# Optimization experiments

Measured on AMD Instinct MI355X. Metric: run time of the kernel, lower is better.

## Reference

```python
import jax, jax.numpy as jnp
import numpy as np

EPS = 1e-7
LN_EPS = 1e-5

# Lorentz model, points represented by spatial coords x in R^dim; time coord t = sqrt(K + ||x||^2), K = 1/c.

def log_map_zero(x, c):
    K = 1.0 / c
    sqrtK = jnp.sqrt(K)
    xnorm = jnp.linalg.norm(x, axis=-1, keepdims=True)
    t = jnp.sqrt(K + xnorm * xnorm)
    theta = jnp.arccosh(jnp.maximum(t / sqrtK, 1.0 + EPS))
    return sqrtK * theta * x / jnp.maximum(xnorm, EPS)


def exp_map_zero(v, c):
    K = 1.0 / c
    sqrtK = jnp.sqrt(K)
    vnorm = jnp.linalg.norm(v, axis=-1, keepdims=True)
    return sqrtK * jnp.sinh(vnorm / sqrtK) * v / jnp.maximum(vnorm, EPS)


def layer_norm(x, gamma, beta):
    mu = jnp.mean(x, axis=-1, keepdims=True)
    var = jnp.mean((x - mu) ** 2, axis=-1, keepdims=True)
    return (x - mu) * jax.lax.rsqrt(var + LN_EPS) * gamma + beta


def setup_inputs() -> dict:
    key = jax.random.key(0)
    N, D, E, L = 50000, 128, 800000, 2
    ks = jax.random.split(key, 8)
    x_hyp = jax.random.normal(ks[0], (N, D), dtype=jnp.float32)
    edge_index = jax.random.randint(ks[1], (2, E), 0, N, dtype=jnp.int64)
    W = jax.random.normal(ks[2], (L, D, D), dtype=jnp.float32) / np.sqrt(D)
    b = jnp.zeros((L, D), dtype=jnp.float32)
    gamma = jnp.ones((L, D), dtype=jnp.float32)
    beta = jnp.zeros((L, D), dtype=jnp.float32)
    curv = jnp.ones((L,), dtype=jnp.float32)
    return {"x_hyp": x_hyp, "edge_index": edge_index, "W": W, "b": b,
            "gamma": gamma, "beta": beta, "curv": curv}


def reference(x_hyp, edge_index, W, b, gamma, beta, curv):
    N = x_hyp.shape[0]
    L = W.shape[0]
    src, dst = edge_index[0], edge_index[1]
    # in-degree counts for mean aggregation (clamped to avoid div by 0)
    counts = jax.ops.segment_sum(jnp.ones_like(dst, dtype=x_hyp.dtype), dst, num_segments=N)
    counts = jnp.maximum(counts, 1.0)[:, None]
    x = x_hyp
    for l in range(L):
        # curvature treated as constant (torch uses .item())
        c = jax.lax.stop_gradient(jnp.clip(curv[l], 0.1, 10.0))
        x_tan = log_map_zero(x, c)                      # [N, D]
        x_lin = x_tan @ W[l].T + b[l]                   # [N, D]
        msgs = x_lin[src]                               # [E, D] gather
        agg = jax.ops.segment_sum(msgs, dst, num_segments=N) / counts  # scatter-mean
        x_tan_out = layer_norm(x_tan + agg, gamma[l], beta[l])  # dropout in eval mode
        x = exp_map_zero(x_tan_out, c)
    return x
```

## Files before the change

kernel.cpp:

```cpp
#include <hip/hip_runtime.h>
#include <hip/hip_bf16.h>

typedef __attribute__((ext_vector_type(4))) float f32x4;
typedef __attribute__((ext_vector_type(2))) float f32x2;
typedef __attribute__((ext_vector_type(8))) short bf16x8;

constexpr int D = 128;
constexpr int SB = 256;
constexpr int K4CAP = 8192;
#define FEPS 1e-7f
#define FLN_EPS 1e-5f

__device__ __forceinline__ float groupReduceSum16(float x) {
#pragma unroll
  for (int off = 1; off < 16; off <<= 1) x += __shfl_xor(x, off, 64);
  return x;
}

__device__ __forceinline__ unsigned short f2bf(float x) {
  unsigned int u = __float_as_uint(x);
  u += 0x7fffu + ((u >> 16) & 1u);
  return (unsigned short)(u >> 16);
}

__device__ __forceinline__ unsigned int pack2(float a, float b) {
  return (unsigned int)f2bf(a) | ((unsigned int)f2bf(b) << 16);
}

__device__ __forceinline__ f32x2 unp(unsigned int x) {
  f32x2 r;
  r.x = __uint_as_float(x << 16);
  r.y = __uint_as_float(x & 0xffff0000u);
  return r;
}

struct AccSet {
  f32x2 e0, o0, e1, o1;
};

__device__ __forceinline__ void accu(AccSet& s, uint4 u) {
  f32x2 t;
  t.x = __uint_as_float(u.x << 16);
  t.y = __uint_as_float(u.y << 16);
  s.e0 += t;
  t.x = __uint_as_float(u.x);
  t.y = __uint_as_float(u.y);
  s.o0 += t;
  t.x = __uint_as_float(u.z << 16);
  t.y = __uint_as_float(u.w << 16);
  s.e1 += t;
  t.x = __uint_as_float(u.z);
  t.y = __uint_as_float(u.w);
  s.o1 += t;
}


__global__ __launch_bounds__(1024) void k2_scan(int* __restrict__ bh,
                                                int* __restrict__ bucket_base, int NB, int E) {
  __shared__ int bsum[256];
  int tid = threadIdx.x, lane = tid & 63, wv = tid >> 6;
  for (int bin = wv; bin < NB; bin += 16) {
    int carry = 0;
    int* row = bh + bin * SB;
#pragma unroll
    for (int sgm = 0; sgm < 4; ++sgm) {
      int v = row[sgm * 64 + lane];
      int x = v;
#pragma unroll
      for (int off = 1; off < 64; off <<= 1) {
        int t = __shfl_up(x, off, 64);
        if (lane >= off) x += t;
      }
      row[sgm * 64 + lane] = carry + x - v;
      carry += __shfl(x, 63, 64);
    }
    if (lane == 0) bsum[bin] = carry;
  }
  __syncthreads();
  if (wv == 0) {
    int carry = 0;
    for (int base = 0; base < NB; base += 64) {
      int v = (base + lane < NB) ? bsum[base + lane] : 0;
      int x = v;
#pragma unroll
      for (int off = 1; off < 64; off <<= 1) {
        int t = __shfl_up(x, off, 64);
        if (lane >= off) x += t;
      }
      if (base + lane < NB) {
        int excl = carry + x - v;
        bsum[base + lane] = excl;
        bucket_base[base + lane] = excl;
      }
      carry += __shfl(x, 63, 64);
    }
    if (lane == 0) bucket_base[NB] = E;
  }
  __syncthreads();
  for (int bin = wv; bin < NB; bin += 16) {
    int bb = bsum[bin];
    int* row = bh + bin * SB;
    for (int s = lane; s < SB; s += 64) row[s] += bb;
  }
}

__global__ __launch_bounds__(1024) void k3_scatter(const int* __restrict__ src,
                                                   const int* __restrict__ dst,
                                                   const int* __restrict__ bh,
                                                   unsigned int* __restrict__ ebuf, int E,
                                                   int NB, int chunk) {
  __shared__ int base[256];
  __shared__ int cur[256];
  int tid = threadIdx.x;
  if (tid < 256) {
    base[tid] = (tid < NB) ? bh[tid * SB + blockIdx.x] : 0;
    cur[tid] = 0;
  }
  __syncthreads();
  int e0 = blockIdx.x * chunk;
  int e1 = min(e0 + chunk, E);
  for (int e = e0 + tid; e < e1; e += 1024) {
    int d = dst[e];
    int s = src[e];
    int bin = d >> 8;
    int r = atomicAdd(&cur[bin], 1);
    ebuf[base[bin] + r] = (unsigned int)(s & 0xffff) | ((unsigned int)(d & 255) << 16);
  }
}

__global__ __launch_bounds__(1024) void k4_csr(const unsigned int* __restrict__ ebuf,
                                               const int* __restrict__ bucket_base,
                                               int* __restrict__ rowptr,
                                               unsigned short* __restrict__ col, int N, int NB,
                                               int E) {
  __shared__ unsigned int stash[K4CAP];
  __shared__ int hist[256];
  __shared__ int cur[256];
  int b = blockIdx.x, tid = threadIdx.x;
  int e0 = bucket_base[b], e1 = bucket_base[b + 1];
  int cnt = e1 - e0;
  if (tid < 256) {
    hist[tid] = 0;
    cur[tid] = 0;
  }
  __syncthreads();
  for (int i = tid; i < cnt; i += 1024) {
    unsigned int u = ebuf[e0 + i];
    if (i < K4CAP) stash[i] = u;
    atomicAdd(&hist[u >> 16], 1);
  }
  __syncthreads();
  int lane = tid & 63;
  if (tid < 64) {
    int carry = 0;
#pragma unroll
    for (int sgm = 0; sgm < 4; ++sgm) {
      int v = hist[sgm * 64 + lane];
      int x = v;
#pragma unroll
      for (int off = 1; off < 64; off <<= 1) {
        int t = __shfl_up(x, off, 64);
        if (lane >= off) x += t;
      }
      hist[sgm * 64 + lane] = carry + x - v;
      carry += __shfl(x, 63, 64);
    }
  }
  __syncthreads();
  int node0 = b << 8;
  if (tid < 256 && node0 + tid < N) rowptr[node0 + tid] = e0 + hist[tid];
  if (b == 0 && tid == 0) rowptr[N] = E;
  for (int i = tid; i < cnt; i += 1024) {
    unsigned int u = (i < K4CAP) ? stash[i] : ebuf[e0 + i];
    int slot = u >> 16;
    int r = atomicAdd(&cur[slot], 1);
    col[e0 + hist[slot] + r] = (unsigned short)(u & 0xffff);
  }
}


__device__ __forceinline__ void gemm0_body(int gbid, unsigned short* Wlds,
                                           const float* __restrict__ xf,
                                           const float* __restrict__ Wf,
                                           const float* __restrict__ bias,
                                           const float* __restrict__ curv,
                                           unsigned short* __restrict__ xt,
                                           unsigned short* __restrict__ xl, int N) {
  const float* Wp = Wf;
  for (int idx = threadIdx.x; idx < 2048; idx += 1024) {
    int lanei = idx & 63, kbt = idx >> 6;
    int kb = kbt & 3, tcol = kbt >> 2;
    int g = lanei >> 4, r = lanei & 15;
    const float* s = Wp + (size_t)(tcol * 16 + r) * D + kb * 32 + g * 8;
    float4 f0 = *reinterpret_cast<const float4*>(s);
    float4 f1 = *reinterpret_cast<const float4*>(s + 4);
    uint4 u;
    u.x = pack2(f0.x, f0.y);
    u.y = pack2(f0.z, f0.w);
    u.z = pack2(f1.x, f1.y);
    u.w = pack2(f1.z, f1.w);
    *reinterpret_cast<uint4*>(&Wlds[idx * 8]) = u;
  }
  __syncthreads();
  int lane = threadIdx.x & 63;
  int trow = gbid * 16 + (threadIdx.x >> 6);
  int n0 = trow * 16;
  if (n0 >= N) return;
  int g = lane >> 4, r = lane & 15;
  int ar = n0 + r;
  if (ar > N - 1) ar = N - 1;

  bf16x8 af[4];
  float c = fminf(fmaxf(curv[0], 0.1f), 10.0f);
  float K = 1.0f / c, sqrtK = sqrtf(K);
  float4 fa[4][2];
  float ss = 0.f;
#pragma unroll
  for (int kb = 0; kb < 4; ++kb) {
    const float4* xr = reinterpret_cast<const float4*>(xf + (size_t)ar * D + kb * 32 + g * 8);
    fa[kb][0] = xr[0];
    fa[kb][1] = xr[1];
    ss += fa[kb][0].x * fa[kb][0].x + fa[kb][0].y * fa[kb][0].y + fa[kb][0].z * fa[kb][0].z +
          fa[kb][0].w * fa[kb][0].w;
    ss += fa[kb][1].x * fa[kb][1].x + fa[kb][1].y * fa[kb][1].y + fa[kb][1].z * fa[kb][1].z +
          fa[kb][1].w * fa[kb][1].w;
  }
  ss += __shfl_xor(ss, 16, 64);
  ss += __shfl_xor(ss, 32, 64);
  float xnorm = sqrtf(ss);
  float t = sqrtf(K + ss);
  float theta = acoshf(fmaxf(t / sqrtK, 1.0f + FEPS));
  float scale = sqrtK * theta / fmaxf(xnorm, FEPS);
#pragma unroll
  for (int kb = 0; kb < 4; ++kb) {
    union { bf16x8 v; uint4 u; } cv;
    cv.u.x = pack2(fa[kb][0].x * scale, fa[kb][0].y * scale);
    cv.u.y = pack2(fa[kb][0].z * scale, fa[kb][0].w * scale);
    cv.u.z = pack2(fa[kb][1].x * scale, fa[kb][1].y * scale);
    cv.u.w = pack2(fa[kb][1].z * scale, fa[kb][1].w * scale);
    af[kb] = cv.v;
    *reinterpret_cast<uint4*>(xt + (size_t)ar * D + kb * 32 + g * 8) = cv.u;
  }

  int colj = lane & 15, rb = (lane >> 4) * 4;
#pragma unroll
  for (int tcol = 0; tcol < 8; ++tcol) {
    f32x4 acc = {0.f, 0.f, 0.f, 0.f};
#pragma unroll
    for (int kb = 0; kb < 4; ++kb) {
      bf16x8 bfm = *reinterpret_cast<const bf16x8*>(&Wlds[((tcol * 4 + kb) * 64 + lane) * 8]);
      acc = __builtin_amdgcn_mfma_f32_16x16x32_bf16(af[kb], bfm, acc, 0, 0, 0);
    }
    float bv = bias[tcol * 16 + colj];
#pragma unroll
    for (int i = 0; i < 4; ++i) {
      int row = n0 + rb + i;
      if (row < N) xl[(size_t)row * D + tcol * 16 + colj] = f2bf(acc[i] + bv);
    }
  }
}

__global__ __launch_bounds__(1024) void fusedA_kernel(const int* __restrict__ dst,
                                                      int* __restrict__ bh, int E, int NB,
                                                      int chunk, const float* __restrict__ xf,
                                                      const float* __restrict__ Wf,
                                                      const float* __restrict__ bias,
                                                      const float* __restrict__ curv,
                                                      unsigned short* __restrict__ xt,
                                                      unsigned short* __restrict__ xl, int N,
                                                      unsigned short* __restrict__ W16,
                                                      int nconv, int gblocks) {
  __shared__ unsigned short Wlds[128 * 128];
  int bid = blockIdx.x;
  if (bid < SB) {
    int* h = (int*)Wlds;
    int tid = threadIdx.x;
    if (tid < 256) h[tid] = 0;
    __syncthreads();
    int e0 = bid * chunk;
    int e1 = min(e0 + chunk, E);
    for (int e = e0 + tid; e < e1; e += 1024) atomicAdd(&h[dst[e] >> 8], 1);
    __syncthreads();
    if (tid < NB) bh[tid * SB + bid] = h[tid];
  } else if (bid < SB + gblocks) {
    gemm0_body(bid - SB, Wlds, xf, Wf, bias, curv, xt, xl, N);
  } else {
    for (int i = threadIdx.x * 4; i < nconv; i += 4096) {
      float4 f = *reinterpret_cast<const float4*>(Wf + D * D + i);
      uint2 o;
      o.x = pack2(f.x, f.y);
      o.y = pack2(f.z, f.w);
      *reinterpret_cast<uint2*>(W16 + i) = o;
    }
  }
}


template <int MODE>
__global__ __launch_bounds__(256) void agg_kernel(const unsigned short* __restrict__ xl_in,
                                                  unsigned short* __restrict__ xt,
                                                  const int* __restrict__ rowptr,
                                                  const unsigned short* __restrict__ col,
                                                  const float* __restrict__ gamma,
                                                  const float* __restrict__ beta,
                                                  const float* __restrict__ curv, int l,
                                                  const unsigned short* __restrict__ W16n,
                                                  const float* __restrict__ bias,
                                                  unsigned short* __restrict__ xl_out,
                                                  float* __restrict__ out, int N) {
  __shared__ unsigned short xtile[16 * 136];
  int tid = threadIdx.x;
  int lane = tid & 63;
  int gl = lane & 15, g = lane >> 4;
  int wid = tid >> 6;
  int node = blockIdx.x * 16 + wid * 4 + g;
  bool active = node < N;
  int nd = active ? node : N - 1;

  float c = fminf(fmaxf(curv[l], 0.1f), 10.0f);
  float K = 1.0f / c, sqrtK = sqrtf(K);

  int e0 = rowptr[nd], e1 = rowptr[nd + 1];
  int deg = e1 - e0;
  const unsigned short* cb = col + e0;

  AccSet S[4];
#pragma unroll
  for (int j = 0; j < 4; ++j) {
    S[j].e0 = 0.f;
    S[j].o0 = 0.f;
    S[j].e1 = 0.f;
    S[j].o1 = 0.f;
  }

  const uint4* xlp = reinterpret_cast<const uint4*>(xl_in);
  for (int base = 0; base < deg; base += 16) {
    int cidx = (base + gl < deg) ? (int)cb[base + gl] : 0;
    int m = deg - base;
    if (m > 16) m = 16;
    int k = 0;
    for (; k + 8 <= m; k += 8) {
      uint4 u[8];
#pragma unroll
      for (int t = 0; t < 8; ++t) {
        int s = __shfl(cidx, g * 16 + k + t, 64);
        u[t] = xlp[(size_t)s * 16 + gl];
      }
#pragma unroll
      for (int t = 0; t < 8; ++t) accu(S[t & 3], u[t]);
    }
    for (; k + 2 <= m; k += 2) {
      int s0 = __shfl(cidx, g * 16 + k, 64);
      int s1 = __shfl(cidx, g * 16 + k + 1, 64);
      uint4 u0 = xlp[(size_t)s0 * 16 + gl];
      uint4 u1 = xlp[(size_t)s1 * 16 + gl];
      accu(S[0], u0);
      accu(S[1], u1);
    }
    if (k < m) {
      int s0 = __shfl(cidx, g * 16 + k, 64);
      uint4 u0 = xlp[(size_t)s0 * 16 + gl];
      accu(S[0], u0);
    }
  }
  f32x2 E0 = (S[0].e0 + S[1].e0) + (S[2].e0 + S[3].e0);
  f32x2 O0 = (S[0].o0 + S[1].o0) + (S[2].o0 + S[3].o0);
  f32x2 E1 = (S[0].e1 + S[1].e1) + (S[2].e1 + S[3].e1);
  f32x2 O1 = (S[0].o1 + S[1].o1) + (S[2].o1 + S[3].o1);
  float a[8] = {E0.x, O0.x, E0.y, O0.y, E1.x, O1.x, E1.y, O1.y};

  float inv = 1.f / fmaxf((float)deg, 1.f);
  uint4 ut = reinterpret_cast<const uint4*>(xt)[(size_t)nd * 16 + gl];
  f32x2 utv[4];
  utv[0] = unp(ut.x);
  utv[1] = unp(ut.y);
  utv[2] = unp(ut.z);
  utv[3] = unp(ut.w);
  float v[8];
#pragma unroll
  for (int j = 0; j < 4; ++j) {
    v[2 * j] = utv[j].x + a[2 * j] * inv;
    v[2 * j + 1] = utv[j].y + a[2 * j + 1] * inv;
  }

  float s1 = 0.f, s2 = 0.f;
#pragma unroll
  for (int j = 0; j < 8; ++j) {
    s1 += v[j];
    s2 += v[j] * v[j];
  }
  s1 = groupReduceSum16(s1);
  s2 = groupReduceSum16(s2);
  float mu = s1 * (1.f / 128.f);
  float var = fmaxf(s2 * (1.f / 128.f) - mu * mu, 0.f);
  float rstd = rsqrtf(var + FLN_EPS);

  float4 gm0 = *reinterpret_cast<const float4*>(gamma + l * D + gl * 8);
  float4 gm1 = *reinterpret_cast<const float4*>(gamma + l * D + gl * 8 + 4);
  float4 bt0 = *reinterpret_cast<const float4*>(beta + l * D + gl * 8);
  float4 bt1 = *reinterpret_cast<const float4*>(beta + l * D + gl * 8 + 4);
  float y[8];
  y[0] = (v[0] - mu) * rstd * gm0.x + bt0.x;
  y[1] = (v[1] - mu) * rstd * gm0.y + bt0.y;
  y[2] = (v[2] - mu) * rstd * gm0.z + bt0.z;
  y[3] = (v[3] - mu) * rstd * gm0.w + bt0.w;
  y[4] = (v[4] - mu) * rstd * gm1.x + bt1.x;
  y[5] = (v[5] - mu) * rstd * gm1.y + bt1.y;
  y[6] = (v[6] - mu) * rstd * gm1.z + bt1.z;
  y[7] = (v[7] - mu) * rstd * gm1.w + bt1.w;

  float ss = 0.f;
#pragma unroll
  for (int j = 0; j < 8; ++j) ss += y[j] * y[j];
  ss = groupReduceSum16(ss);
  float vn = sqrtf(ss);
  float sc = sqrtK * sinhf(vn / sqrtK) / fmaxf(vn, FEPS);

  if (MODE == 0) {
    if (active) {
      float4 o0, o1;
      o0.x = y[0] * sc;
      o0.y = y[1] * sc;
      o0.z = y[2] * sc;
      o0.w = y[3] * sc;
      o1.x = y[4] * sc;
      o1.y = y[5] * sc;
      o1.z = y[6] * sc;
      o1.w = y[7] * sc;
      float4* op = reinterpret_cast<float4*>(out + (size_t)node * D + gl * 8);
      op[0] = o0;
      op[1] = o1;
    }
  } else {
    float xn = sqrtK * sinhf(vn / sqrtK);
    float c2 = fminf(fmaxf(curv[l + 1], 0.1f), 10.0f);
    float K2 = 1.0f / c2, sqrtK2 = sqrtf(K2);
    float t2 = sqrtf(K2 + xn * xn);
    float theta = acoshf(fmaxf(t2 / sqrtK2, 1.0f + FEPS));
    float sc2 = sqrtK2 * theta / fmaxf(xn, FEPS);
    float st = sc * sc2;
    uint4 w;
    w.x = pack2(y[0] * st, y[1] * st);
    w.y = pack2(y[2] * st, y[3] * st);
    w.z = pack2(y[4] * st, y[5] * st);
    w.w = pack2(y[6] * st, y[7] * st);
    int noderow = wid * 4 + g;
    *reinterpret_cast<uint4*>(&xtile[noderow * 136 + gl * 8]) = w;
    if (active) reinterpret_cast<uint4*>(xt)[(size_t)node * 16 + gl] = w;
    __syncthreads();

    int rr = lane & 15, kg = lane >> 4;
    bf16x8 af[4];
#pragma unroll
    for (int kb = 0; kb < 4; ++kb)
      af[kb] = *reinterpret_cast<const bf16x8*>(&xtile[rr * 136 + kb * 32 + kg * 8]);
    int n0 = blockIdx.x * 16;
    int rb = kg * 4;
#pragma unroll
    for (int t = 0; t < 2; ++t) {
      int tcol = wid * 2 + t;
      f32x4 acc = {0.f, 0.f, 0.f, 0.f};
#pragma unroll
      for (int kb = 0; kb < 4; ++kb) {
        bf16x8 bfm = *reinterpret_cast<const bf16x8*>(W16n + (size_t)(tcol * 16 + rr) * D +
                                                      kb * 32 + kg * 8);
        acc = __builtin_amdgcn_mfma_f32_16x16x32_bf16(af[kb], bfm, acc, 0, 0, 0);
      }
      float bv = bias[(l + 1) * D + tcol * 16 + rr];
#pragma unroll
      for (int i = 0; i < 4; ++i) {
        int row = n0 + rb + i;
        if (row < N) xl_out[(size_t)row * D + tcol * 16 + rr] = f2bf(acc[i] + bv);
      }
    }
  }
}


extern "C" void kernel_launch(void* const* d_in, const int* in_sizes, int n_in,
                              void* d_out, int out_size, void* d_ws, size_t ws_size,
                              hipStream_t stream) {
  const float* x_hyp = (const float*)d_in[0];
  const int* edge = (const int*)d_in[1];
  const float* W = (const float*)d_in[2];
  const float* b = (const float*)d_in[3];
  const float* gamma = (const float*)d_in[4];
  const float* beta = (const float*)d_in[5];
  const float* curv = (const float*)d_in[6];
  float* out = (float*)d_out;
  int N = in_sizes[0] / D;
  int E = in_sizes[1] / 2;
  int L = in_sizes[6];
  const int* src = edge;
  const int* dst = edge + E;

  char* p = (char*)d_ws;
  auto alloc = [&](size_t bytes) {
    char* r = p;
    p += (bytes + 255) & ~(size_t)255;
    return r;
  };
  int NB = (N + 255) >> 8;
  int chunk = (E + SB - 1) / SB;

  int* bh = (int*)alloc((size_t)256 * SB * 4);
  int* bucket_base = (int*)alloc((size_t)(NB + 1) * 4);
  unsigned int* ebuf = (unsigned int*)alloc((size_t)E * 4);
  int* rowptr = (int*)alloc((size_t)(N + 1) * 4);
  unsigned short* colp = (unsigned short*)alloc((size_t)E * 2);
  unsigned short* xt16 = (unsigned short*)alloc((size_t)N * D * 2);
  unsigned short* xlA = (unsigned short*)alloc((size_t)N * D * 2);
  unsigned short* xlB = (unsigned short*)alloc((size_t)N * D * 2);
  unsigned short* W16 = (unsigned short*)alloc((size_t)(L > 1 ? (L - 1) : 1) * D * D * 2);

  int g1024 = ((N + 15) / 16 + 15) / 16;
  int nconv = (L - 1) * D * D;

  fusedA_kernel<<<SB + g1024 + 1, 1024, 0, stream>>>(dst, bh, E, NB, chunk, x_hyp, W, b, curv,
                                                     xt16, xlA, N, W16, nconv, g1024);
  k2_scan<<<1, 1024, 0, stream>>>(bh, bucket_base, NB, E);
  k3_scatter<<<SB, 1024, 0, stream>>>(src, dst, bh, ebuf, E, NB, chunk);
  k4_csr<<<NB, 1024, 0, stream>>>(ebuf, bucket_base, rowptr, colp, N, NB, E);

  unsigned short* xl_cur = xlA;
  unsigned short* xl_nxt = xlB;
  for (int l = 0; l < L; ++l) {
    if (l < L - 1) {
      agg_kernel<1><<<(N + 15) / 16, 256, 0, stream>>>(
          xl_cur, xt16, rowptr, colp, gamma, beta, curv, l, W16 + (size_t)l * D * D, b, xl_nxt,
          out, N);
      unsigned short* tmp = xl_cur;
      xl_cur = xl_nxt;
      xl_nxt = tmp;
    } else {
      agg_kernel<0><<<(N + 15) / 16, 256, 0, stream>>>(xl_cur, xt16, rowptr, colp, gamma, beta,
                                                       curv, l, nullptr, b, nullptr, out, N);
    }
  }
}
```

Before: 149.6 us.

## Split layer GEMM out of aggregation kernel and rebundle CSR build stages

The layer-1 GEMM is moved out of the aggregation kernel into a separate MFMA kernel that stages W in LDS, so the aggregation kernel no longer needs a shared tile or a block barrier. The histogram pass becomes its own kernel, and the edge scatter now runs concurrently with the layer-0 GEMM in one bundled launch. The gather loop is reworked to prefetch the next batch of column indices and to use 4-wide unrolling with two accumulator sets instead of 8-wide with four. This adds one extra kernel launch and a global round trip of xt between aggregation and GEMM, in exchange for lower register and LDS pressure in the aggregation kernel.

```diff
diff --git a/kernel.cpp b/kernel.cpp
--- a/kernel.cpp
+++ b/kernel.cpp
@@ -55,6 +55,19 @@
 }
 
 
+__global__ __launch_bounds__(1024) void k1_hist(const int* __restrict__ dst,
+                                                int* __restrict__ bh, int E, int NB, int chunk) {
+  __shared__ int h[256];
+  int tid = threadIdx.x;
+  if (tid < 256) h[tid] = 0;
+  __syncthreads();
+  int e0 = blockIdx.x * chunk;
+  int e1 = min(e0 + chunk, E);
+  for (int e = e0 + tid; e < e1; e += 1024) atomicAdd(&h[dst[e] >> 8], 1);
+  __syncthreads();
+  if (tid < NB) bh[tid * SB + blockIdx.x] = h[tid];
+}
+
 __global__ __launch_bounds__(1024) void k2_scan(int* __restrict__ bh,
                                                 int* __restrict__ bucket_base, int NB, int E) {
   __shared__ int bsum[256];
@@ -101,30 +114,6 @@
     int bb = bsum[bin];
     int* row = bh + bin * SB;
     for (int s = lane; s < SB; s += 64) row[s] += bb;
-  }
-}
-
-__global__ __launch_bounds__(1024) void k3_scatter(const int* __restrict__ src,
-                                                   const int* __restrict__ dst,
-                                                   const int* __restrict__ bh,
-                                                   unsigned int* __restrict__ ebuf, int E,
-                                                   int NB, int chunk) {
-  __shared__ int base[256];
-  __shared__ int cur[256];
-  int tid = threadIdx.x;
-  if (tid < 256) {
-    base[tid] = (tid < NB) ? bh[tid * SB + blockIdx.x] : 0;
-    cur[tid] = 0;
-  }
-  __syncthreads();
-  int e0 = blockIdx.x * chunk;
-  int e1 = min(e0 + chunk, E);
-  for (int e = e0 + tid; e < e1; e += 1024) {
-    int d = dst[e];
-    int s = src[e];
-    int bin = d >> 8;
-    int r = atomicAdd(&cur[bin], 1);
-    ebuf[base[bin] + r] = (unsigned int)(s & 0xffff) | ((unsigned int)(d & 255) << 16);
   }
 }
 
@@ -186,12 +175,11 @@
                                            const float* __restrict__ curv,
                                            unsigned short* __restrict__ xt,
                                            unsigned short* __restrict__ xl, int N) {
-  const float* Wp = Wf;
   for (int idx = threadIdx.x; idx < 2048; idx += 1024) {
     int lanei = idx & 63, kbt = idx >> 6;
     int kb = kbt & 3, tcol = kbt >> 2;
     int g = lanei >> 4, r = lanei & 15;
-    const float* s = Wp + (size_t)(tcol * 16 + r) * D + kb * 32 + g * 8;
+    const float* s = Wf + (size_t)(tcol * 16 + r) * D + kb * 32 + g * 8;
     float4 f0 = *reinterpret_cast<const float4*>(s);
     float4 f1 = *reinterpret_cast<const float4*>(s + 4);
     uint4 u;
@@ -260,28 +248,33 @@
   }
 }
 
-__global__ __launch_bounds__(1024) void fusedA_kernel(const int* __restrict__ dst,
-                                                      int* __restrict__ bh, int E, int NB,
-                                                      int chunk, const float* __restrict__ xf,
-                                                      const float* __restrict__ Wf,
-                                                      const float* __restrict__ bias,
-                                                      const float* __restrict__ curv,
-                                                      unsigned short* __restrict__ xt,
-                                                      unsigned short* __restrict__ xl, int N,
-                                                      unsigned short* __restrict__ W16,
-                                                      int nconv, int gblocks) {
+__global__ __launch_bounds__(1024) void bundle_kernel(
+    const int* __restrict__ src, const int* __restrict__ dst, const int* __restrict__ bh,
+    unsigned int* __restrict__ ebuf, int E, int NB, int chunk, const float* __restrict__ xf,
+    const float* __restrict__ Wf, const float* __restrict__ bias,
+    const float* __restrict__ curv, unsigned short* __restrict__ xt,
+    unsigned short* __restrict__ xl, int N, unsigned short* __restrict__ W16, int nconv,
+    int gblocks) {
   __shared__ unsigned short Wlds[128 * 128];
   int bid = blockIdx.x;
   if (bid < SB) {
-    int* h = (int*)Wlds;
+    int* base = (int*)Wlds;
+    int* cur = base + 256;
     int tid = threadIdx.x;
-    if (tid < 256) h[tid] = 0;
+    if (tid < 256) {
+      base[tid] = (tid < NB) ? bh[tid * SB + bid] : 0;
+      cur[tid] = 0;
+    }
     __syncthreads();
     int e0 = bid * chunk;
     int e1 = min(e0 + chunk, E);
-    for (int e = e0 + tid; e < e1; e += 1024) atomicAdd(&h[dst[e] >> 8], 1);
-    __syncthreads();
-    if (tid < NB) bh[tid * SB + bid] = h[tid];
+    for (int e = e0 + tid; e < e1; e += 1024) {
+      int d = dst[e];
+      int s = src[e];
+      int bin = d >> 8;
+      int r = atomicAdd(&cur[bin], 1);
+      ebuf[base[bin] + r] = (unsigned int)(s & 0xffff) | ((unsigned int)(d & 255) << 16);
+    }
   } else if (bid < SB + gblocks) {
     gemm0_body(bid - SB, Wlds, xf, Wf, bias, curv, xt, xl, N);
   } else {
@@ -296,6 +289,50 @@
 }
 
 
+__global__ __launch_bounds__(1024) void gemm_kernel(const unsigned short* __restrict__ A,
+                                                    const unsigned short* __restrict__ W16,
+                                                    const float* __restrict__ bias, int l,
+                                                    unsigned short* __restrict__ xl, int N) {
+  __shared__ unsigned short Wlds[128 * 128];
+  const unsigned short* Wp = W16 + (size_t)(l - 1) * D * D;
+  for (int idx = threadIdx.x; idx < 2048; idx += 1024) {
+    int lanei = idx & 63, kbt = idx >> 6;
+    int kb = kbt & 3, tcol = kbt >> 2;
+    int g = lanei >> 4, r = lanei & 15;
+    *reinterpret_cast<uint4*>(&Wlds[idx * 8]) =
+        *reinterpret_cast<const uint4*>(Wp + (size_t)(tcol * 16 + r) * D + kb * 32 + g * 8);
+  }
+  __syncthreads();
+  int lane = threadIdx.x & 63;
+  int trow = blockIdx.x * 16 + (threadIdx.x >> 6);
+  int n0 = trow * 16;
+  if (n0 >= N) return;
+  int g = lane >> 4, r = lane & 15;
+  int ar = n0 + r;
+  if (ar > N - 1) ar = N - 1;
+  bf16x8 af[4];
+#pragma unroll
+  for (int kb = 0; kb < 4; ++kb)
+    af[kb] = *reinterpret_cast<const bf16x8*>(A + (size_t)ar * D + kb * 32 + g * 8);
+  int colj = lane & 15, rb = (lane >> 4) * 4;
+#pragma unroll
+  for (int tcol = 0; tcol < 8; ++tcol) {
+    f32x4 acc = {0.f, 0.f, 0.f, 0.f};
+#pragma unroll
+    for (int kb = 0; kb < 4; ++kb) {
+      bf16x8 bfm = *reinterpret_cast<const bf16x8*>(&Wlds[((tcol * 4 + kb) * 64 + lane) * 8]);
+      acc = __builtin_amdgcn_mfma_f32_16x16x32_bf16(af[kb], bfm, acc, 0, 0, 0);
+    }
+    float bv = bias[l * D + tcol * 16 + colj];
+#pragma unroll
+    for (int i = 0; i < 4; ++i) {
+      int row = n0 + rb + i;
+      if (row < N) xl[(size_t)row * D + tcol * 16 + colj] = f2bf(acc[i] + bv);
+    }
+  }
+}
+
+
 template <int MODE>
 __global__ __launch_bounds__(256) void agg_kernel(const unsigned short* __restrict__ xl_in,
                                                   unsigned short* __restrict__ xt,
@@ -304,11 +341,7 @@
                                                   const float* __restrict__ gamma,
                                                   const float* __restrict__ beta,
                                                   const float* __restrict__ curv, int l,
-                                                  const unsigned short* __restrict__ W16n,
-                                                  const float* __restrict__ bias,
-                                                  unsigned short* __restrict__ xl_out,
                                                   float* __restrict__ out, int N) {
-  __shared__ unsigned short xtile[16 * 136];
   int tid = threadIdx.x;
   int lane = tid & 63;
   int gl = lane & 15, g = lane >> 4;
@@ -324,49 +357,43 @@
   int deg = e1 - e0;
   const unsigned short* cb = col + e0;
 
-  AccSet S[4];
-#pragma unroll
-  for (int j = 0; j < 4; ++j) {
-    S[j].e0 = 0.f;
-    S[j].o0 = 0.f;
-    S[j].e1 = 0.f;
-    S[j].o1 = 0.f;
-  }
+  AccSet S0, S1;
+  S0.e0 = 0.f; S0.o0 = 0.f; S0.e1 = 0.f; S0.o1 = 0.f;
+  S1.e0 = 0.f; S1.o0 = 0.f; S1.e1 = 0.f; S1.o1 = 0.f;
 
   const uint4* xlp = reinterpret_cast<const uint4*>(xl_in);
+  int cidx = (gl < deg) ? (int)cb[gl] : 0;
   for (int base = 0; base < deg; base += 16) {
-    int cidx = (base + gl < deg) ? (int)cb[base + gl] : 0;
+    int nb = base + 16;
+    int cnext = (nb + gl < deg) ? (int)cb[nb + gl] : 0;
     int m = deg - base;
     if (m > 16) m = 16;
     int k = 0;
-    for (; k + 8 <= m; k += 8) {
-      uint4 u[8];
-#pragma unroll
-      for (int t = 0; t < 8; ++t) {
-        int s = __shfl(cidx, g * 16 + k + t, 64);
-        u[t] = xlp[(size_t)s * 16 + gl];
-      }
-#pragma unroll
-      for (int t = 0; t < 8; ++t) accu(S[t & 3], u[t]);
-    }
-    for (; k + 2 <= m; k += 2) {
+    for (; k + 4 <= m; k += 4) {
       int s0 = __shfl(cidx, g * 16 + k, 64);
       int s1 = __shfl(cidx, g * 16 + k + 1, 64);
+      int s2 = __shfl(cidx, g * 16 + k + 2, 64);
+      int s3 = __shfl(cidx, g * 16 + k + 3, 64);
       uint4 u0 = xlp[(size_t)s0 * 16 + gl];
       uint4 u1 = xlp[(size_t)s1 * 16 + gl];
-      accu(S[0], u0);
-      accu(S[1], u1);
-    }
-    if (k < m) {
+      uint4 u2 = xlp[(size_t)s2 * 16 + gl];
+      uint4 u3 = xlp[(size_t)s3 * 16 + gl];
+      accu(S0, u0);
+      accu(S1, u1);
+      accu(S0, u2);
+      accu(S1, u3);
+    }
+    for (; k < m; ++k) {
       int s0 = __shfl(cidx, g * 16 + k, 64);
       uint4 u0 = xlp[(size_t)s0 * 16 + gl];
-      accu(S[0], u0);
-    }
-  }
-  f32x2 E0 = (S[0].e0 + S[1].e0) + (S[2].e0 + S[3].e0);
-  f32x2 O0 = (S[0].o0 + S[1].o0) + (S[2].o0 + S[3].o0);
-  f32x2 E1 = (S[0].e1 + S[1].e1) + (S[2].e1 + S[3].e1);
-  f32x2 O1 = (S[0].o1 + S[1].o1) + (S[2].o1 + S[3].o1);
+      accu(S0, u0);
+    }
+    cidx = cnext;
+  }
+  f32x2 E0 = S0.e0 + S1.e0;
+  f32x2 O0 = S0.o0 + S1.o0;
+  f32x2 E1 = S0.e1 + S1.e1;
+  f32x2 O1 = S0.o1 + S1.o1;
   float a[8] = {E0.x, O0.x, E0.y, O0.y, E1.x, O1.x, E1.y, O1.y};
 
   float inv = 1.f / fmaxf((float)deg, 1.f);
@@ -439,39 +466,13 @@
     float theta = acoshf(fmaxf(t2 / sqrtK2, 1.0f + FEPS));
     float sc2 = sqrtK2 * theta / fmaxf(xn, FEPS);
     float st = sc * sc2;
-    uint4 w;
-    w.x = pack2(y[0] * st, y[1] * st);
-    w.y = pack2(y[2] * st, y[3] * st);
-    w.z = pack2(y[4] * st, y[5] * st);
-    w.w = pack2(y[6] * st, y[7] * st);
-    int noderow = wid * 4 + g;
-    *reinterpret_cast<uint4*>(&xtile[noderow * 136 + gl * 8]) = w;
-    if (active) reinterpret_cast<uint4*>(xt)[(size_t)node * 16 + gl] = w;
-    __syncthreads();
-
-    int rr = lane & 15, kg = lane >> 4;
-    bf16x8 af[4];
-#pragma unroll
-    for (int kb = 0; kb < 4; ++kb)
-      af[kb] = *reinterpret_cast<const bf16x8*>(&xtile[rr * 136 + kb * 32 + kg * 8]);
-    int n0 = blockIdx.x * 16;
-    int rb = kg * 4;
-#pragma unroll
-    for (int t = 0; t < 2; ++t) {
-      int tcol = wid * 2 + t;
-      f32x4 acc = {0.f, 0.f, 0.f, 0.f};
-#pragma unroll
-      for (int kb = 0; kb < 4; ++kb) {
-        bf16x8 bfm = *reinterpret_cast<const bf16x8*>(W16n + (size_t)(tcol * 16 + rr) * D +
-                                                      kb * 32 + kg * 8);
-        acc = __builtin_amdgcn_mfma_f32_16x16x32_bf16(af[kb], bfm, acc, 0, 0, 0);
-      }
-      float bv = bias[(l + 1) * D + tcol * 16 + rr];
-#pragma unroll
-      for (int i = 0; i < 4; ++i) {
-        int row = n0 + rb + i;
-        if (row < N) xl_out[(size_t)row * D + tcol * 16 + rr] = f2bf(acc[i] + bv);
-      }
+    if (active) {
+      uint4 w;
+      w.x = pack2(y[0] * st, y[1] * st);
+      w.y = pack2(y[2] * st, y[3] * st);
+      w.z = pack2(y[4] * st, y[5] * st);
+      w.w = pack2(y[6] * st, y[7] * st);
+      reinterpret_cast<uint4*>(xt)[(size_t)node * 16 + gl] = w;
     }
   }
 }
@@ -516,25 +517,26 @@
   int g1024 = ((N + 15) / 16 + 15) / 16;
   int nconv = (L - 1) * D * D;
 
-  fusedA_kernel<<<SB + g1024 + 1, 1024, 0, stream>>>(dst, bh, E, NB, chunk, x_hyp, W, b, curv,
-                                                     xt16, xlA, N, W16, nconv, g1024);
+  k1_hist<<<SB, 1024, 0, stream>>>(dst, bh, E, NB, chunk);
   k2_scan<<<1, 1024, 0, stream>>>(bh, bucket_base, NB, E);
-  k3_scatter<<<SB, 1024, 0, stream>>>(src, dst, bh, ebuf, E, NB, chunk);
+  bundle_kernel<<<SB + g1024 + 1, 1024, 0, stream>>>(src, dst, bh, ebuf, E, NB, chunk, x_hyp,
+                                                     W, b, curv, xt16, xlA, N, W16, nconv,
+                                                     g1024);
   k4_csr<<<NB, 1024, 0, stream>>>(ebuf, bucket_base, rowptr, colp, N, NB, E);
 
   unsigned short* xl_cur = xlA;
   unsigned short* xl_nxt = xlB;
   for (int l = 0; l < L; ++l) {
     if (l < L - 1) {
-      agg_kernel<1><<<(N + 15) / 16, 256, 0, stream>>>(
-          xl_cur, xt16, rowptr, colp, gamma, beta, curv, l, W16 + (size_t)l * D * D, b, xl_nxt,
-          out, N);
+      agg_kernel<1><<<(N + 15) / 16, 256, 0, stream>>>(xl_cur, xt16, rowptr, colp, gamma, beta,
+                                                       curv, l, out, N);
+      gemm_kernel<<<g1024, 1024, 0, stream>>>(xt16, W16, b, l + 1, xl_nxt, N);
       unsigned short* tmp = xl_cur;
       xl_cur = xl_nxt;
       xl_nxt = tmp;
     } else {
       agg_kernel<0><<<(N + 15) / 16, 256, 0, stream>>>(xl_cur, xt16, rowptr, colp, gamma, beta,
-                                                       curv, l, nullptr, b, nullptr, out, N);
-    }
-  }
-}
+                                                       curv, l, out, N);
+    }
+  }
+}
```

Result: faster. 140.9 us, median of 2 (-5.9%).
